# Kernel tuning notes

Measured on AMD Instinct MI355X. Metric: run time of the kernel, lower is better.

The kernel has to match this reference:

```python
import jax, jax.numpy as jnp
import numpy as np

B, S, E, H, BS = 4, 4096, 1024, 1024, 128  # batch, seq, embed, head_size, block_size


def setup_inputs() -> dict:
    key = jax.random.key(0)
    k1, k2, k3, k4 = jax.random.split(key, 4)
    x = jax.random.normal(k1, (B, S, E), dtype=jnp.float32)
    W_qkv = jax.random.normal(k2, (E, 3 * H), dtype=jnp.float32) * (E ** -0.5)
    W_out = jax.random.normal(k3, (H, H), dtype=jnp.float32) * (H ** -0.5)
    b_out = jax.random.normal(k4, (H,), dtype=jnp.float32) * 0.01
    return {"x": x, "W_qkv": W_qkv, "W_out": W_out, "b_out": b_out}


def reference(x, W_qkv, W_out, b_out):
    b, s, e = x.shape
    h = W_out.shape[1]
    nb = s // BS  # number of blocks (block-diagonal attention)
    qkv = x @ W_qkv                      # [B, S, 3H]
    q, k, v = jnp.split(qkv, 3, axis=-1)

    def blk(t):
        return t.reshape(b, nb, BS, h)   # [B, nb, BS, H]

    scale = h ** -0.5
    # each query block attends only its own key/value block
    scores = jnp.einsum('bnqd,bnkd->bnqk', blk(q), blk(k)) * scale  # [B, nb, BS, BS]
    causal = jnp.tril(jnp.ones((BS, BS), dtype=bool))  # diagonal block of full tril
    scores = jnp.where(causal, scores, -jnp.inf)
    scores = scores - jnp.max(scores, axis=-1, keepdims=True)
    p = jnp.exp(scores)
    p = p / (jnp.sum(p, axis=-1, keepdims=True) + 1e-6)  # faithful: softmax with +1e-6 eps
    out = jnp.einsum('bnqk,bnkd->bnqd', p, blk(v)).reshape(b, s, h)
    return out @ W_out.T + b_out
```

## Files before the change

kernel.cpp:

```cpp
#include <hip/hip_runtime.h>
#include <hip/hip_bf16.h>

typedef __attribute__((ext_vector_type(8))) short short8;
typedef __attribute__((ext_vector_type(4))) float float4_;

__device__ __forceinline__ short f2b(float f) {
  union { __hip_bfloat16 h; short s; } u;
  u.h = __float2bfloat16(f);
  return u.s;
}
__device__ __forceinline__ float b2f(short s) {
  union { short s; __hip_bfloat16 h; } u;
  u.s = s;
  return __bfloat162float(u.h);
}
__device__ __forceinline__ short8 cvt8(float4_ lo, float4_ hi) {
  short8 r;
#pragma unroll
  for (int t = 0; t < 4; t++) { r[t] = f2b(lo[t]); r[t + 4] = f2b(hi[t]); }
  return r;
}

__global__ __launch_bounds__(256) void f32_to_b16(
    const float* __restrict__ in, short* __restrict__ out, long n)
{
  const long i = ((long)blockIdx.x * 256 + threadIdx.x) * 8;
  if (i >= n) return;
  float4_ lo = *(const float4_*)&in[i];
  float4_ hi = *(const float4_*)&in[i + 4];
  *(short8*)&out[i] = cvt8(lo, hi);
}

__global__ __launch_bounds__(256) void transpose64(
    const float* __restrict__ in, short* __restrict__ out, int R, int C)
{
  __shared__ __align__(16) short T[64 * 72];
  const int tid = threadIdx.x;
  const int r0 = blockIdx.y * 64;
  const int c0 = blockIdx.x * 64;
  const int r  = tid >> 2;
  const int cp = (tid & 3) * 16;
#pragma unroll
  for (int g = 0; g < 4; g++) {
    float4_ v = *(const float4_*)&in[(long)(r0 + r) * C + c0 + cp + g * 4];
#pragma unroll
    for (int t = 0; t < 4; t++) T[(cp + g * 4 + t) * 72 + r] = f2b(v[t]);
  }
  __syncthreads();
  const int c  = tid >> 2;
  const int rp = (tid & 3) * 16;
  short8 w0 = *(const short8*)&T[c * 72 + rp];
  short8 w1 = *(const short8*)&T[c * 72 + rp + 8];
  *(short8*)&out[(long)(c0 + c) * R + r0 + rp] = w0;
  *(short8*)&out[(long)(c0 + c) * R + r0 + rp + 8] = w1;
}

__global__ __launch_bounds__(256) void gemm_bt(
    const void* __restrict__ Av, int lda, int a_f32,
    const short* __restrict__ B,
    void* __restrict__ Cv, int ldc, int c_f32,
    int K, const float* __restrict__ bias)
{
  __shared__ __align__(16) short As[128 * 32];
  __shared__ __align__(16) short Bs[128 * 32];
  const int tid  = threadIdx.x;
  const int lane = tid & 63;
  const int w    = tid >> 6;
  const int quad = lane >> 4;
  const int l15  = lane & 15;
  const int wm   = (w >> 1) * 64;
  const int wn   = (w & 1) * 64;
  const int m0   = blockIdx.y * 128;
  const int n0   = blockIdx.x * 128;

  float4_ acc[4][4] = {};

  const int srow = tid >> 2;
  const int kp   = (tid & 3) * 8;

  for (int k0 = 0; k0 < K; k0 += 32) {
    short8 a_lo, a_hi;
    if (a_f32) {
      const float* Af = (const float*)Av;
      float4_ l0 = *(const float4_*)&Af[(long)(m0 + srow) * lda + k0 + kp];
      float4_ l1 = *(const float4_*)&Af[(long)(m0 + srow) * lda + k0 + kp + 4];
      float4_ h0 = *(const float4_*)&Af[(long)(m0 + srow + 64) * lda + k0 + kp];
      float4_ h1 = *(const float4_*)&Af[(long)(m0 + srow + 64) * lda + k0 + kp + 4];
      a_lo = cvt8(l0, l1);
      a_hi = cvt8(h0, h1);
    } else {
      const short* As_ = (const short*)Av;
      a_lo = *(const short8*)&As_[(long)(m0 + srow) * lda + k0 + kp];
      a_hi = *(const short8*)&As_[(long)(m0 + srow + 64) * lda + k0 + kp];
    }
    short8 b_lo = *(const short8*)&B[(long)(n0 + srow) * K + k0 + kp];
    short8 b_hi = *(const short8*)&B[(long)(n0 + srow + 64) * K + k0 + kp];
    __syncthreads();
    *(short8*)&As[srow * 32 + kp]        = a_lo;
    *(short8*)&As[(srow + 64) * 32 + kp] = a_hi;
    *(short8*)&Bs[srow * 32 + kp]        = b_lo;
    *(short8*)&Bs[(srow + 64) * 32 + kp] = b_hi;
    __syncthreads();
    short8 a[4], b[4];
#pragma unroll
    for (int i = 0; i < 4; i++)
      a[i] = *(const short8*)&As[(wm + i * 16 + l15) * 32 + quad * 8];
#pragma unroll
    for (int j = 0; j < 4; j++)
      b[j] = *(const short8*)&Bs[(wn + j * 16 + l15) * 32 + quad * 8];
#pragma unroll
    for (int i = 0; i < 4; i++)
#pragma unroll
      for (int j = 0; j < 4; j++)
        acc[i][j] = __builtin_amdgcn_mfma_f32_16x16x32_bf16(a[i], b[j], acc[i][j], 0, 0, 0);
  }

#pragma unroll
  for (int i = 0; i < 4; i++) {
    const int rm = m0 + wm + i * 16 + quad * 4;
#pragma unroll
    for (int j = 0; j < 4; j++) {
      const int cn = n0 + wn + j * 16 + l15;
      if (c_f32) {
        float* C = (float*)Cv;
        const float bv = bias ? bias[cn] : 0.0f;
#pragma unroll
        for (int r = 0; r < 4; r++)
          C[(long)(rm + r) * ldc + cn] = acc[i][j][r] + bv;
      } else {
        short* C = (short*)Cv;
#pragma unroll
        for (int r = 0; r < 4; r++)
          C[(long)(rm + r) * ldc + cn] = f2b(acc[i][j][r]);
      }
    }
  }
}

__global__ __launch_bounds__(256) void attn_blockdiag(short* __restrict__ qkv)
{
  __shared__ __align__(16) short Qs[128 * 32];
  __shared__ __align__(16) short Ks[128 * 32];
  __shared__ __align__(16) short Ps[128 * 136];

  const int tid  = threadIdx.x;
  const int lane = tid & 63;
  const int w    = tid >> 6;
  const int quad = lane >> 4;
  const int l15  = lane & 15;
  const long base = (long)blockIdx.x * 128 * 3072;

  float4_ acc[2][8] = {};
  const int srow = tid >> 2;
  const int kp   = (tid & 3) * 8;
  const short* Qg = qkv + base;
  const short* Kg = qkv + base + 1024;

  for (int k0 = 0; k0 < 1024; k0 += 32) {
    short8 q_lo = *(const short8*)&Qg[(long)srow * 3072 + k0 + kp];
    short8 q_hi = *(const short8*)&Qg[(long)(srow + 64) * 3072 + k0 + kp];
    short8 k_lo = *(const short8*)&Kg[(long)srow * 3072 + k0 + kp];
    short8 k_hi = *(const short8*)&Kg[(long)(srow + 64) * 3072 + k0 + kp];
    __syncthreads();
    *(short8*)&Qs[srow * 32 + kp]        = q_lo;
    *(short8*)&Qs[(srow + 64) * 32 + kp] = q_hi;
    *(short8*)&Ks[srow * 32 + kp]        = k_lo;
    *(short8*)&Ks[(srow + 64) * 32 + kp] = k_hi;
    __syncthreads();
    short8 a0 = *(const short8*)&Qs[(w * 32 + l15) * 32 + quad * 8];
    short8 a1 = *(const short8*)&Qs[(w * 32 + 16 + l15) * 32 + quad * 8];
#pragma unroll
    for (int j = 0; j < 8; j++) {
      short8 b = *(const short8*)&Ks[(j * 16 + l15) * 32 + quad * 8];
      acc[0][j] = __builtin_amdgcn_mfma_f32_16x16x32_bf16(a0, b, acc[0][j], 0, 0, 0);
      acc[1][j] = __builtin_amdgcn_mfma_f32_16x16x32_bf16(a1, b, acc[1][j], 0, 0, 0);
    }
  }
  __syncthreads();

  const float scale = 0.03125f;
#pragma unroll
  for (int i = 0; i < 2; i++) {
#pragma unroll
    for (int r = 0; r < 4; r++) {
      const int rowq = w * 32 + i * 16 + quad * 4 + r;
      float s[8];
      float mx = -3.0e38f;
#pragma unroll
      for (int j = 0; j < 8; j++) {
        const int col = j * 16 + l15;
        const float v = acc[i][j][r] * scale;
        s[j] = (col <= rowq) ? v : -3.0e38f;
        mx = fmaxf(mx, s[j]);
      }
      mx = fmaxf(mx, __shfl_xor(mx, 1));
      mx = fmaxf(mx, __shfl_xor(mx, 2));
      mx = fmaxf(mx, __shfl_xor(mx, 4));
      mx = fmaxf(mx, __shfl_xor(mx, 8));
      float p[8];
      float sum = 0.0f;
#pragma unroll
      for (int j = 0; j < 8; j++) {
        p[j] = (s[j] > -1.0e38f) ? __expf(s[j] - mx) : 0.0f;
        sum += p[j];
      }
      sum += __shfl_xor(sum, 1);
      sum += __shfl_xor(sum, 2);
      sum += __shfl_xor(sum, 4);
      sum += __shfl_xor(sum, 8);
      const float inv = 1.0f / (sum + 1e-6f);
#pragma unroll
      for (int j = 0; j < 8; j++)
        Ps[rowq * 136 + j * 16 + l15] = f2b(p[j] * inv);
    }
  }
  __syncthreads();

  const short* Vg = qkv + base + 2048;
  short* Op = qkv + base;
  for (int d0 = 0; d0 < 1024; d0 += 64) {
    float4_ o[2][4] = {};
#pragma unroll
    for (int kk = 0; kk < 4; kk++) {
      short8 a0 = *(const short8*)&Ps[(w * 32 + l15) * 136 + kk * 32 + quad * 8];
      short8 a1 = *(const short8*)&Ps[(w * 32 + 16 + l15) * 136 + kk * 32 + quad * 8];
      const int kb = kk * 32 + quad * 8;
#pragma unroll
      for (int j = 0; j < 4; j++) {
        const int d = d0 + j * 16 + l15;
        short8 b;
#pragma unroll
        for (int t = 0; t < 8; t++)
          b[t] = Vg[(long)(kb + t) * 3072 + d];
        o[0][j] = __builtin_amdgcn_mfma_f32_16x16x32_bf16(a0, b, o[0][j], 0, 0, 0);
        o[1][j] = __builtin_amdgcn_mfma_f32_16x16x32_bf16(a1, b, o[1][j], 0, 0, 0);
      }
    }
#pragma unroll
    for (int i = 0; i < 2; i++)
#pragma unroll
      for (int j = 0; j < 4; j++)
#pragma unroll
        for (int r = 0; r < 4; r++) {
          const int rq = w * 32 + i * 16 + quad * 4 + r;
          const int d  = d0 + j * 16 + l15;
          Op[(long)rq * 3072 + d] = f2b(o[i][j][r]);
        }
  }
}

extern "C" void kernel_launch(void* const* d_in, const int* in_sizes, int n_in,
                              void* d_out, int out_size, void* d_ws, size_t ws_size,
                              hipStream_t stream) {
  const float* x    = (const float*)d_in[0];
  const float* Wqkv = (const float*)d_in[1];
  const float* Wout = (const float*)d_in[2];
  const float* bout = (const float*)d_in[3];
  float* out = (float*)d_out;

  char* ws = (char*)d_ws;
  short* WqkvT = (short*)ws;
  short* Woutb = (short*)(ws + 6291456);
  short* qkv   = (short*)(ws + 8388608);
  short* xb    = (short*)(ws + 8388608 + (size_t)16384 * 3072 * 2);

  transpose64<<<dim3(48, 16), 256, 0, stream>>>(Wqkv, WqkvT, 1024, 3072);
  f32_to_b16<<<512, 256, 0, stream>>>(Wout, Woutb, 1048576L);

  if (ws_size >= 8388608 + (size_t)16384 * 3072 * 2 + (size_t)16384 * 1024 * 2) {
    f32_to_b16<<<8192, 256, 0, stream>>>(x, xb, 16777216L);
    gemm_bt<<<dim3(24, 128), 256, 0, stream>>>(xb, 1024, 0, WqkvT,
                                               qkv, 3072, 0, 1024, nullptr);
    attn_blockdiag<<<dim3(128), 256, 0, stream>>>(qkv);
    gemm_bt<<<dim3(8, 128), 256, 0, stream>>>(qkv, 3072, 0, Woutb,
                                              out, 1024, 1, 1024, bout);
  } else if (ws_size >= 8388608 + (size_t)16384 * 3072 * 2) {
    gemm_bt<<<dim3(24, 128), 256, 0, stream>>>(x, 1024, 1, WqkvT,
                                               qkv, 3072, 0, 1024, nullptr);
    attn_blockdiag<<<dim3(128), 256, 0, stream>>>(qkv);
    gemm_bt<<<dim3(8, 128), 256, 0, stream>>>(qkv, 3072, 0, Woutb,
                                              out, 1024, 1, 1024, bout);
  } else {
    for (int c = 0; c < 4; c++) {
      const float* xc = x + (long)c * 4096 * 1024;
      float* outc = out + (long)c * 4096 * 1024;
      gemm_bt<<<dim3(24, 32), 256, 0, stream>>>(xc, 1024, 1, WqkvT,
                                                qkv, 3072, 0, 1024, nullptr);
      attn_blockdiag<<<dim3(32), 256, 0, stream>>>(qkv);
      gemm_bt<<<dim3(8, 32), 256, 0, stream>>>(qkv, 3072, 0, Woutb,
                                               outc, 1024, 1, 1024, bout);
    }
  }
}
```

Baseline: 385.5 us.

## Use direct global-to-LDS loads and stage transposed V tiles in shared memory

Replaces the register-staged global loads of the bf16 A/B tiles in the GEMM and of Q/K in the attention kernel with global_load_lds 16-byte direct-to-LDS transfers. These rely on the per-wave contiguous layout matching the row-major tile. In the PV phase, each 128x64 V tile is now loaded cooperatively with vector loads and transposed into an LDS buffer. This replaces strided scalar global gathers per MFMA operand. The transpose writes are scalar and may cause LDS bank conflicts, and there are extra barriers per d-chunk.

```diff
diff --git a/kernel.cpp b/kernel.cpp
--- a/kernel.cpp
+++ b/kernel.cpp
@@ -3,6 +3,13 @@
 
 typedef __attribute__((ext_vector_type(8))) short short8;
 typedef __attribute__((ext_vector_type(4))) float float4_;
+
+typedef const __attribute__((address_space(1))) void* gas_t;
+typedef __attribute__((address_space(3))) void* las_t;
+
+__device__ __forceinline__ void gl_lds16(const void* g, void* l) {
+  __builtin_amdgcn_global_load_lds((gas_t)g, (las_t)l, 16, 0, 0);
+}
 
 __device__ __forceinline__ short f2b(float f) {
   union { __hip_bfloat16 h; short s; } u;
@@ -72,6 +79,7 @@
   const int wn   = (w & 1) * 64;
   const int m0   = blockIdx.y * 128;
   const int n0   = blockIdx.x * 128;
+  const int wbase = w * 512;
 
   float4_ acc[4][4] = {};
 
@@ -88,18 +96,18 @@
       float4_ h1 = *(const float4_*)&Af[(long)(m0 + srow + 64) * lda + k0 + kp + 4];
       a_lo = cvt8(l0, l1);
       a_hi = cvt8(h0, h1);
+    }
+    __syncthreads();
+    if (a_f32) {
+      *(short8*)&As[srow * 32 + kp]        = a_lo;
+      *(short8*)&As[(srow + 64) * 32 + kp] = a_hi;
     } else {
-      const short* As_ = (const short*)Av;
-      a_lo = *(const short8*)&As_[(long)(m0 + srow) * lda + k0 + kp];
-      a_hi = *(const short8*)&As_[(long)(m0 + srow + 64) * lda + k0 + kp];
-    }
-    short8 b_lo = *(const short8*)&B[(long)(n0 + srow) * K + k0 + kp];
-    short8 b_hi = *(const short8*)&B[(long)(n0 + srow + 64) * K + k0 + kp];
-    __syncthreads();
-    *(short8*)&As[srow * 32 + kp]        = a_lo;
-    *(short8*)&As[(srow + 64) * 32 + kp] = a_hi;
-    *(short8*)&Bs[srow * 32 + kp]        = b_lo;
-    *(short8*)&Bs[(srow + 64) * 32 + kp] = b_hi;
+      const short* Ab = (const short*)Av;
+      gl_lds16(&Ab[(long)(m0 + srow) * lda + k0 + kp],      &As[wbase]);
+      gl_lds16(&Ab[(long)(m0 + srow + 64) * lda + k0 + kp], &As[2048 + wbase]);
+    }
+    gl_lds16(&B[(long)(n0 + srow) * K + k0 + kp],      &Bs[wbase]);
+    gl_lds16(&B[(long)(n0 + srow + 64) * K + k0 + kp], &Bs[2048 + wbase]);
     __syncthreads();
     short8 a[4], b[4];
 #pragma unroll
@@ -142,6 +150,7 @@
   __shared__ __align__(16) short Qs[128 * 32];
   __shared__ __align__(16) short Ks[128 * 32];
   __shared__ __align__(16) short Ps[128 * 136];
+  __shared__ __align__(16) short Vt[64 * 136];
 
   const int tid  = threadIdx.x;
   const int lane = tid & 63;
@@ -149,6 +158,7 @@
   const int quad = lane >> 4;
   const int l15  = lane & 15;
   const long base = (long)blockIdx.x * 128 * 3072;
+  const int wbase = w * 512;
 
   float4_ acc[2][8] = {};
   const int srow = tid >> 2;
@@ -157,15 +167,11 @@
   const short* Kg = qkv + base + 1024;
 
   for (int k0 = 0; k0 < 1024; k0 += 32) {
-    short8 q_lo = *(const short8*)&Qg[(long)srow * 3072 + k0 + kp];
-    short8 q_hi = *(const short8*)&Qg[(long)(srow + 64) * 3072 + k0 + kp];
-    short8 k_lo = *(const short8*)&Kg[(long)srow * 3072 + k0 + kp];
-    short8 k_hi = *(const short8*)&Kg[(long)(srow + 64) * 3072 + k0 + kp];
-    __syncthreads();
-    *(short8*)&Qs[srow * 32 + kp]        = q_lo;
-    *(short8*)&Qs[(srow + 64) * 32 + kp] = q_hi;
-    *(short8*)&Ks[srow * 32 + kp]        = k_lo;
-    *(short8*)&Ks[(srow + 64) * 32 + kp] = k_hi;
+    __syncthreads();
+    gl_lds16(&Qg[(long)srow * 3072 + k0 + kp],        &Qs[wbase]);
+    gl_lds16(&Qg[(long)(srow + 64) * 3072 + k0 + kp], &Qs[2048 + wbase]);
+    gl_lds16(&Kg[(long)srow * 3072 + k0 + kp],        &Ks[wbase]);
+    gl_lds16(&Kg[(long)(srow + 64) * 3072 + k0 + kp], &Ks[2048 + wbase]);
     __syncthreads();
     short8 a0 = *(const short8*)&Qs[(w * 32 + l15) * 32 + quad * 8];
     short8 a1 = *(const short8*)&Qs[(w * 32 + 16 + l15) * 32 + quad * 8];
@@ -214,11 +220,23 @@
         Ps[rowq * 136 + j * 16 + l15] = f2b(p[j] * inv);
     }
   }
-  __syncthreads();
 
   const short* Vg = qkv + base + 2048;
   short* Op = qkv + base;
+  const int kr = tid >> 1;
+  const int dp = (tid & 1) * 32;
+
   for (int d0 = 0; d0 < 1024; d0 += 64) {
+    __syncthreads();
+#pragma unroll
+    for (int g = 0; g < 4; g++) {
+      short8 v = *(const short8*)&Vg[(long)kr * 3072 + d0 + dp + g * 8];
+#pragma unroll
+      for (int t = 0; t < 8; t++)
+        Vt[(dp + g * 8 + t) * 136 + kr] = v[t];
+    }
+    __syncthreads();
+
     float4_ o[2][4] = {};
 #pragma unroll
     for (int kk = 0; kk < 4; kk++) {
@@ -227,11 +245,7 @@
       const int kb = kk * 32 + quad * 8;
 #pragma unroll
       for (int j = 0; j < 4; j++) {
-        const int d = d0 + j * 16 + l15;
-        short8 b;
-#pragma unroll
-        for (int t = 0; t < 8; t++)
-          b[t] = Vg[(long)(kb + t) * 3072 + d];
+        short8 b = *(const short8*)&Vt[(j * 16 + l15) * 136 + kb];
         o[0][j] = __builtin_amdgcn_mfma_f32_16x16x32_bf16(a0, b, o[0][j], 0, 0, 0);
         o[1][j] = __builtin_amdgcn_mfma_f32_16x16x32_bf16(a1, b, o[1][j], 0, 0, 0);
       }
```

Measured after the change: 379.9 us. Within noise of the previous version (-1.4%).
